# Kernel optimization log

Measured on AMD Instinct MI355X. Metric: run time of the kernel, lower is better.

## Reference

```python
import jax, jax.numpy as jnp
import numpy as np

N = 100000      # total nodes in batched graph
E = 3200000     # total edges (avg degree 32)
G = 128         # number of graphs in batch
F_IN = 512      # raw node feature dim
NC = 128        # num_classes = projected feature dim (GraphConv layer-0 input)
HID = 256       # hid_channels
OUT = 10        # out_channels
LYR = 3         # args.lyr
EPS = 1e-5      # BatchNorm1d eps


def setup_inputs() -> dict:
    key = jax.random.key(0)
    ks = jax.random.split(key, 20)
    h = jax.random.normal(ks[0], (N, F_IN), dtype=jnp.float32)
    src = jax.random.randint(ks[1], (E,), 0, N, dtype=jnp.int32)
    dst = jax.random.randint(ks[2], (E,), 0, N, dtype=jnp.int32)
    # contiguous sorted graph assignment: every graph non-empty
    graph_ids = (jnp.arange(N, dtype=jnp.int32) * G) // N
    w_init = jax.random.normal(ks[3], (NC, F_IN), dtype=jnp.float32) * 0.05
    inp = dict(h=h, src=src, dst=dst, graph_ids=graph_ids, w_init=w_init)
    dims = [NC, HID, HID]
    for i in range(LYR):
        inp[f"lw{i}"] = jax.random.normal(ks[4 + i], (dims[i], HID), dtype=jnp.float32) * 0.05
        inp[f"lb{i}"] = jnp.zeros((HID,), jnp.float32)
        inp[f"gamma{i}"] = jnp.ones((HID,), jnp.float32)
        inp[f"beta{i}"] = jnp.zeros((HID,), jnp.float32)
    inp["fc_w"] = jax.random.normal(ks[10], (HID, OUT), dtype=jnp.float32) * 0.05
    inp["fc_b"] = jnp.zeros((OUT,), jnp.float32)
    return inp


def _forward(h, src, dst, graph_ids, w_init, layers, fc_w, fc_b):
    # symmetric normalization (DGL GraphConv norm='both')
    ones_e = jnp.ones((E,), h.dtype)
    out_deg = jax.ops.segment_sum(ones_e, src, num_segments=N)
    in_deg = jax.ops.segment_sum(ones_e, dst, num_segments=N)
    norm_src = jnp.where(out_deg > 0, out_deg ** -0.5, 0.0)  # [N]
    norm_dst = jnp.where(in_deg > 0, in_deg ** -0.5, 0.0)    # [N]

    h = h @ w_init.T  # [N, NC]
    for (lw, lb, gamma, beta) in layers:
        # GraphConv: (D_out^-1/2) gather -> scatter-sum -> (D_in^-1/2), then linear
        m = (h * norm_src[:, None])[src]                       # [E, d]
        agg = jax.ops.segment_sum(m, dst, num_segments=N)       # [N, d]
        h = (agg * norm_dst[:, None]) @ lw + lb                 # [N, HID]
        # BatchNorm1d (training-mode batch stats, biased variance) + ReLU
        mu = jnp.mean(h, axis=0)
        var = jnp.mean((h - mu) ** 2, axis=0)
        h = jax.nn.relu((h - mu) * jax.lax.rsqrt(var + EPS) * gamma + beta)
    # dgl.max_nodes: per-graph max over nodes
    hg = jax.ops.segment_max(h, graph_ids, num_segments=G)      # [G, HID]
    return hg @ fc_w + fc_b                                     # [G, OUT]


def reference(h, src, dst, graph_ids, w_init,
              lw0, lb0, gamma0, beta0,
              lw1, lb1, gamma1, beta1,
              lw2, lb2, gamma2, beta2,
              fc_w, fc_b):
    layers = [(lw0, lb0, gamma0, beta0),
              (lw1, lb1, gamma1, beta1),
              (lw2, lb2, gamma2, beta2)]
    return _forward(h, src, dst, graph_ids, w_init, layers, fc_w, fc_b)
```

## Files before the change

kernel.cpp:

```cpp
#include <hip/hip_runtime.h>
#include <hip/hip_bf16.h>

#define N_NODES 100000
#define N_EDGES 3200000
#define N_GRAPHS 128
#define FIN 512
#define NCLS 128
#define HID 256
#define OUT_DIM 10
#define BN_EPS 1e-5f

#define NBUCK 391
#define EPB   ((N_EDGES + NBUCK - 1) / NBUCK)

typedef unsigned short ush;
typedef ush su16x8 __attribute__((ext_vector_type(8)));
typedef ush su16x4 __attribute__((ext_vector_type(4)));
typedef __bf16 bf16x8v __attribute__((ext_vector_type(8)));
typedef float f32x4v __attribute__((ext_vector_type(4)));

__device__ __forceinline__ float bf2f(ush u) {
    union { unsigned int i; float f; } v; v.i = ((unsigned int)u) << 16; return v.f;
}
__device__ __forceinline__ ush f2bf(float f) {
    union { float f; unsigned int i; } v; v.f = f;
    unsigned int r = v.i + 0x7FFFu + ((v.i >> 16) & 1u);
    return (ush)(r >> 16);
}

template <typename T>
__device__ __forceinline__ auto mfma_sel(T a, T b, f32x4v c, int)
    -> decltype(__builtin_amdgcn_mfma_f32_16x16x32_bf16(a, b, c, 0, 0, 0)) {
    return __builtin_amdgcn_mfma_f32_16x16x32_bf16(a, b, c, 0, 0, 0);
}
template <typename T>
__device__ __forceinline__ f32x4v mfma_sel(T a, T b, f32x4v c, long) {
    return __builtin_amdgcn_mfma_f32_16x16x32_bf16(
        __builtin_bit_cast(bf16x8v, a), __builtin_bit_cast(bf16x8v, b), c, 0, 0, 0);
}
__device__ __forceinline__ f32x4v MFMA_BF16(su16x8 a, su16x8 b, f32x4v c) {
    return mfma_sel(a, b, c, 0);
}

__global__ void odeg_kernel(const int* __restrict__ src, int* __restrict__ odeg8) {
    int e = blockIdx.x * 256 + threadIdx.x;
    int c = blockIdx.x & 7;
    if (e < N_EDGES) atomicAdd(&odeg8[(size_t)c * N_NODES + src[e]], 1);
}
__global__ void nsrc_kernel(const int* __restrict__ odeg8, float* __restrict__ nsrc) {
    int n = blockIdx.x * 256 + threadIdx.x;
    if (n < N_NODES) {
        int od = 0;
        #pragma unroll
        for (int c = 0; c < 8; c++) od += odeg8[(size_t)c * N_NODES + n];
        nsrc[n] = od > 0 ? rsqrtf((float)od) : 0.f;
    }
}

__global__ __launch_bounds__(256) void histA_kernel(const int* __restrict__ dst,
                                                    int* __restrict__ hist) {
    __shared__ int hc[NBUCK];
    int tid = threadIdx.x, blk = blockIdx.x;
    for (int i = tid; i < NBUCK; i += 256) hc[i] = 0;
    __syncthreads();
    int e0 = blk * EPB, e1 = e0 + EPB; if (e1 > N_EDGES) e1 = N_EDGES;
    for (int e = e0 + tid; e < e1; e += 256) atomicAdd(&hc[dst[e] >> 8], 1);
    __syncthreads();
    for (int i = tid; i < NBUCK; i += 256) hist[(size_t)blk * NBUCK + i] = hc[i];
}

__global__ __launch_bounds__(512) void bcnt_kernel(const int* __restrict__ hist,
                                                   int* __restrict__ bcnt) {
    __shared__ int ws[8];
    int b = blockIdx.x, tid = threadIdx.x;
    int lane = tid & 63, wid = tid >> 6;
    int v = (tid < NBUCK) ? hist[(size_t)tid * NBUCK + b] : 0;
    #pragma unroll
    for (int off = 32; off > 0; off >>= 1) v += __shfl_down(v, off, 64);
    if (lane == 0) ws[wid] = v;
    __syncthreads();
    if (tid == 0) {
        int s = 0;
        #pragma unroll
        for (int w = 0; w < 8; w++) s += ws[w];
        bcnt[b] = s;
    }
}

__global__ __launch_bounds__(512) void bscan_kernel(const int* __restrict__ bcnt,
                                                    int* __restrict__ bbase) {
    __shared__ int a[512];
    int tid = threadIdx.x;
    int v = (tid < NBUCK) ? bcnt[tid] : 0;
    a[tid] = v;
    __syncthreads();
    for (int s = 1; s < 512; s <<= 1) {
        int y = (tid >= s) ? a[tid - s] : 0;
        __syncthreads();
        a[tid] += y;
        __syncthreads();
    }
    if (tid < NBUCK) bbase[tid] = a[tid] - v;
    if (tid == 0) bbase[NBUCK] = N_EDGES;
}

__global__ __launch_bounds__(512) void boff_kernel(const int* __restrict__ hist,
                                                   const int* __restrict__ bbase,
                                                   int* __restrict__ off) {
    __shared__ int a[512];
    int b = blockIdx.x, tid = threadIdx.x;
    int v = (tid < NBUCK) ? hist[(size_t)tid * NBUCK + b] : 0;
    a[tid] = v;
    __syncthreads();
    for (int s = 1; s < 512; s <<= 1) {
        int y = (tid >= s) ? a[tid - s] : 0;
        __syncthreads();
        a[tid] += y;
        __syncthreads();
    }
    if (tid < NBUCK) off[(size_t)tid * NBUCK + b] = bbase[b] + a[tid] - v;
}

__global__ __launch_bounds__(256) void stage_kernel(const int* __restrict__ src,
                                                    const int* __restrict__ dst,
                                                    const int* __restrict__ off,
                                                    unsigned int* __restrict__ staged) {
    __shared__ int cur[NBUCK];
    int tid = threadIdx.x, blk = blockIdx.x;
    for (int i = tid; i < NBUCK; i += 256) cur[i] = off[(size_t)blk * NBUCK + i];
    __syncthreads();
    int e0 = blk * EPB, e1 = e0 + EPB; if (e1 > N_EDGES) e1 = N_EDGES;
    for (int e = e0 + tid; e < e1; e += 256) {
        int d = dst[e], s = src[e];
        int pos = atomicAdd(&cur[d >> 8], 1);
        staged[pos] = ((unsigned int)(d & 255) << 24) | (unsigned int)s;
    }
}

__global__ __launch_bounds__(256) void csr_kernel(const unsigned int* __restrict__ staged,
                                                  const int* __restrict__ bbase,
                                                  int* __restrict__ roff,
                                                  float* __restrict__ ndst,
                                                  int* __restrict__ csr) {
    __shared__ int cnt[256], pfx[256], cur[256];
    int b = blockIdx.x, tid = threadIdx.x;
    int beg = bbase[b], end = bbase[b + 1];
    int nodeBase = b * 256;
    int nNodes = N_NODES - nodeBase; if (nNodes > 256) nNodes = 256;
    cnt[tid] = 0;
    __syncthreads();
    for (int e = beg + tid; e < end; e += 256) atomicAdd(&cnt[staged[e] >> 24], 1);
    __syncthreads();
    int v = cnt[tid];
    pfx[tid] = v;
    __syncthreads();
    for (int s = 1; s < 256; s <<= 1) {
        int y = (tid >= s) ? pfx[tid - s] : 0;
        __syncthreads();
        pfx[tid] += y;
        __syncthreads();
    }
    int excl = pfx[tid] - v;
    pfx[tid] = excl;
    cur[tid] = 0;
    if (tid < nNodes) {
        int node = nodeBase + tid;
        roff[node] = beg + excl;
        ndst[node] = v > 0 ? rsqrtf((float)v) : 0.f;
    }
    if (b == NBUCK - 1 && tid == 0) roff[N_NODES] = N_EDGES;
    __syncthreads();
    for (int e = beg + tid; e < end; e += 256) {
        unsigned int w = staged[e];
        int dl = w >> 24;
        int pos = beg + pfx[dl] + atomicAdd(&cur[dl], 1);
        csr[pos] = (int)(w & 0xFFFFFFu);
    }
}

__global__ void cvt_w0_kernel(const float* __restrict__ w, ush* __restrict__ o) {
    int i = blockIdx.x * 256 + threadIdx.x;
    if (i < NCLS * FIN) o[i] = f2bf(w[i]);
}
__global__ void cvt_lwT_kernel(const float* __restrict__ lw, ush* __restrict__ o, int K) {
    int i = blockIdx.x * 256 + threadIdx.x;
    if (i < K * HID) {
        int n = i / K, k = i % K;
        o[i] = f2bf(lw[(size_t)k * HID + n]);
    }
}

template <bool A_F32, bool DO_STATS>
__global__ __launch_bounds__(256) void mfma_gemm(
    const void* __restrict__ Aptr, const ush* __restrict__ BT,
    ush* __restrict__ C, int M, int K, int NN,
    const float* __restrict__ rowscale, const float* __restrict__ bias,
    float* __restrict__ stats)
{
    __shared__ __align__(16) ush As[128][40];
    __shared__ __align__(16) ush Bs[128][40];
    const int bn0 = blockIdx.x * 128;
    const int bm0 = blockIdx.y * 128;
    const int tid = threadIdx.x;
    const int lane = tid & 63;
    const int wv = tid >> 6;
    const int wm = (wv >> 1) * 64;
    const int wn = (wv & 1) * 64;
    const int lm = lane & 15;
    const int lg = lane >> 4;

    f32x4v zero = {0.f, 0.f, 0.f, 0.f};
    f32x4v acc[4][4];
    #pragma unroll
    for (int mi = 0; mi < 4; mi++)
        #pragma unroll
        for (int ni = 0; ni < 4; ni++) acc[mi][ni] = zero;

    for (int k0 = 0; k0 < K; k0 += 32) {
        #pragma unroll
        for (int i = 0; i < 2; i++) {
            int seg = tid + i * 256;
            int n = seg >> 2, kp = seg & 3;
            su16x8 v = *(const su16x8*)&BT[(size_t)(bn0 + n) * K + k0 + kp * 8];
            *(su16x8*)&Bs[n][kp * 8] = v;
        }
        if constexpr (A_F32) {
            const float* Af = (const float*)Aptr;
            #pragma unroll
            for (int i = 0; i < 4; i++) {
                int seg = tid + i * 256;
                int m = seg >> 3, kp = seg & 7;
                int gm = bm0 + m; if (gm >= M) gm = M - 1;
                float4 v = *(const float4*)&Af[(size_t)gm * K + k0 + kp * 4];
                su16x4 o = { f2bf(v.x), f2bf(v.y), f2bf(v.z), f2bf(v.w) };
                *(su16x4*)&As[m][kp * 4] = o;
            }
        } else {
            const ush* Ab = (const ush*)Aptr;
            #pragma unroll
            for (int i = 0; i < 2; i++) {
                int seg = tid + i * 256;
                int m = seg >> 2, kp = seg & 3;
                int gm = bm0 + m; if (gm >= M) gm = M - 1;
                su16x8 v = *(const su16x8*)&Ab[(size_t)gm * K + k0 + kp * 8];
                *(su16x8*)&As[m][kp * 8] = v;
            }
        }
        __syncthreads();
        su16x8 af[4], bfr[4];
        #pragma unroll
        for (int i = 0; i < 4; i++)
            af[i] = *(const su16x8*)&As[wm + i * 16 + lm][lg * 8];
        #pragma unroll
        for (int i = 0; i < 4; i++)
            bfr[i] = *(const su16x8*)&Bs[wn + i * 16 + lm][lg * 8];
        #pragma unroll
        for (int mi = 0; mi < 4; mi++)
            #pragma unroll
            for (int ni = 0; ni < 4; ni++)
                acc[mi][ni] = MFMA_BF16(af[mi], bfr[ni], acc[mi][ni]);
        __syncthreads();
    }

    float s4[4] = {0.f, 0.f, 0.f, 0.f}, q4[4] = {0.f, 0.f, 0.f, 0.f};
    #pragma unroll
    for (int mi = 0; mi < 4; mi++) {
        #pragma unroll
        for (int j = 0; j < 4; j++) {
            int gm = bm0 + wm + mi * 16 + lg * 4 + j;
            bool valid = gm < M;
            float rs = (rowscale && valid) ? rowscale[gm] : 1.f;
            #pragma unroll
            for (int ni = 0; ni < 4; ni++) {
                int gn = bn0 + wn + ni * 16 + lm;
                float v = acc[mi][ni][j] * rs;
                if (bias) v += bias[gn];
                if (valid) {
                    C[(size_t)gm * NN + gn] = f2bf(v);
                    if constexpr (DO_STATS) { s4[ni] += v; q4[ni] += v * v; }
                }
            }
        }
    }
    if constexpr (DO_STATS) {
        #pragma unroll
        for (int ni = 0; ni < 4; ni++) {
            s4[ni] += __shfl_xor(s4[ni], 16); s4[ni] += __shfl_xor(s4[ni], 32);
            q4[ni] += __shfl_xor(q4[ni], 16); q4[ni] += __shfl_xor(q4[ni], 32);
        }
        if (lg == 0) {
            #pragma unroll
            for (int ni = 0; ni < 4; ni++) {
                int gn = bn0 + wn + ni * 16 + lm;
                atomicAdd(&stats[gn], s4[ni]);
                atomicAdd(&stats[HID + gn], q4[ni]);
            }
        }
    }
}

__global__ __launch_bounds__(256) void agg128(const ush* __restrict__ hs,
                                              const int* __restrict__ roff,
                                              const int* __restrict__ csr,
                                              ush* __restrict__ out)
{
    int node = (blockIdx.x * 256 + threadIdx.x) >> 6;
    int lane = threadIdx.x & 63;
    if (node >= N_NODES) return;
    int q = lane >> 4;
    int c0 = (lane & 15) * 8;
    int beg = roff[node], end = roff[node + 1];
    float accA[8] = {}, accB[8] = {};
    int e = beg + q;
    for (; e + 4 < end; e += 8) {
        int s0 = __builtin_nontemporal_load(&csr[e]);
        int s1 = __builtin_nontemporal_load(&csr[e + 4]);
        su16x8 v0 = *(const su16x8*)&hs[(size_t)s0 * 128 + c0];
        su16x8 v1 = *(const su16x8*)&hs[(size_t)s1 * 128 + c0];
        #pragma unroll
        for (int j = 0; j < 8; j++) { accA[j] += bf2f(v0[j]); accB[j] += bf2f(v1[j]); }
    }
    if (e < end) {
        int s0 = __builtin_nontemporal_load(&csr[e]);
        su16x8 v0 = *(const su16x8*)&hs[(size_t)s0 * 128 + c0];
        #pragma unroll
        for (int j = 0; j < 8; j++) accA[j] += bf2f(v0[j]);
    }
    #pragma unroll
    for (int j = 0; j < 8; j++) {
        accA[j] += accB[j];
        accA[j] += __shfl_xor(accA[j], 16);
        accA[j] += __shfl_xor(accA[j], 32);
    }
    if (lane < 16) {
        su16x8 o;
        #pragma unroll
        for (int j = 0; j < 8; j++) o[j] = f2bf(accA[j]);
        __builtin_nontemporal_store(o, (su16x8*)&out[(size_t)node * 128 + c0]);
    }
}

__global__ __launch_bounds__(256) void agg256(const ush* __restrict__ Q,
                                              const int* __restrict__ roff,
                                              const int* __restrict__ csr,
                                              ush* __restrict__ out)
{
    int node = (blockIdx.x * 256 + threadIdx.x) >> 6;
    int lane = threadIdx.x & 63;
    if (node >= N_NODES) return;
    int half = lane >> 5;
    int c0 = (lane & 31) * 8;
    int beg = roff[node], end = roff[node + 1];
    float accA[8] = {}, accB[8] = {};
    int e = beg + half;
    for (; e + 2 < end; e += 4) {
        int s0 = __builtin_nontemporal_load(&csr[e]);
        int s1 = __builtin_nontemporal_load(&csr[e + 2]);
        su16x8 v0 = *(const su16x8*)&Q[(size_t)s0 * 256 + c0];
        su16x8 v1 = *(const su16x8*)&Q[(size_t)s1 * 256 + c0];
        #pragma unroll
        for (int j = 0; j < 8; j++) { accA[j] += bf2f(v0[j]); accB[j] += bf2f(v1[j]); }
    }
    if (e < end) {
        int s0 = __builtin_nontemporal_load(&csr[e]);
        su16x8 v0 = *(const su16x8*)&Q[(size_t)s0 * 256 + c0];
        #pragma unroll
        for (int j = 0; j < 8; j++) accA[j] += bf2f(v0[j]);
    }
    #pragma unroll
    for (int j = 0; j < 8; j++) {
        accA[j] += accB[j];
        accA[j] += __shfl_xor(accA[j], 32);
    }
    if (lane < 32) {
        su16x8 o;
        #pragma unroll
        for (int j = 0; j < 8; j++) o[j] = f2bf(accA[j]);
        __builtin_nontemporal_store(o, (su16x8*)&out[(size_t)node * 256 + c0]);
    }
}

__global__ __launch_bounds__(256) void bnq_kernel(const ush* __restrict__ P,
                                                  const float* __restrict__ stats,
                                                  const float* __restrict__ gamma,
                                                  const float* __restrict__ beta,
                                                  const float* __restrict__ nsrc,
                                                  ush* __restrict__ Q)
{
    __shared__ float sa[HID], sb[HID];
    int tid = threadIdx.x;
    {
        const float inv_n = 1.f / (float)N_NODES;
        float mu = stats[tid] * inv_n;
        float var = fmaf(-mu, mu, stats[HID + tid] * inv_n);
        float a = gamma[tid] * rsqrtf(var + BN_EPS);
        sa[tid] = a;
        sb[tid] = fmaf(-mu, a, beta[tid]);
    }
    __syncthreads();
    const int total = N_NODES * 32;
    for (int idx = blockIdx.x * 256 + tid; idx < total; idx += gridDim.x * 256) {
        int r = idx >> 5, c0 = (idx & 31) * 8;
        su16x8 v = __builtin_nontemporal_load((const su16x8*)&P[(size_t)r * HID + c0]);
        float ns = nsrc[r];
        su16x8 o;
        #pragma unroll
        for (int j = 0; j < 8; j++) {
            float x = fmaxf(fmaf(bf2f(v[j]), sa[c0 + j], sb[c0 + j]), 0.f) * ns;
            o[j] = f2bf(x);
        }
        *(su16x8*)&Q[(size_t)r * HID + c0] = o;
    }
}

__global__ void gstart_kernel(const int* __restrict__ gids, int* __restrict__ gstart) {
    int n = blockIdx.x * 256 + threadIdx.x;
    if (n >= N_NODES) return;
    int g = gids[n];
    int gp = (n == 0) ? -1 : gids[n - 1];
    for (int gg = gp + 1; gg <= g; gg++) gstart[gg] = n;
    if (n == N_NODES - 1) {
        for (int gg = g + 1; gg <= N_GRAPHS; gg++) gstart[gg] = N_NODES;
    }
}

__global__ __launch_bounds__(256) void segmax_ab(const ush* __restrict__ pre,
                                                 const float* __restrict__ stats,
                                                 const float* __restrict__ gamma,
                                                 const float* __restrict__ beta,
                                                 const int* __restrict__ gstart,
                                                 float* __restrict__ hg) {
    int c = threadIdx.x;
    const float inv_n = 1.f / (float)N_NODES;
    float mu = stats[c] * inv_n;
    float var = fmaf(-mu, mu, stats[HID + c] * inv_n);
    float a = gamma[c] * rsqrtf(var + BN_EPS);
    float b = fmaf(-mu, a, beta[c]);
    int g = blockIdx.x;
    int chunk = blockIdx.y;
    int beg = gstart[g], end = gstart[g + 1];
    int len = end - beg;
    int per = (len + 7) >> 3;
    int s = beg + chunk * per;
    int e = s + per; if (e > end) e = end;
    float m0 = 0.f, m1 = 0.f;
    int n = s;
    for (; n + 1 < e; n += 2) {
        m0 = fmaxf(m0, fmaf(bf2f(pre[(size_t)n * HID + c]), a, b));
        m1 = fmaxf(m1, fmaf(bf2f(pre[(size_t)(n + 1) * HID + c]), a, b));
    }
    if (n < e) m0 = fmaxf(m0, fmaf(bf2f(pre[(size_t)n * HID + c]), a, b));
    float m = fmaxf(fmaxf(m0, m1), 0.f);
    atomicMax((int*)&hg[g * HID + c], __float_as_int(m));
}

__global__ void fc_kernel(const float* __restrict__ hg, const float* __restrict__ w,
                          const float* __restrict__ b, float* __restrict__ out) {
    int idx = blockIdx.x * 256 + threadIdx.x;
    if (idx >= N_GRAPHS * OUT_DIM) return;
    int g = idx / OUT_DIM, j = idx % OUT_DIM;
    float s = b[j];
    for (int c = 0; c < HID; c++) s += hg[g * HID + c] * w[c * OUT_DIM + j];
    out[idx] = s;
}

extern "C" void kernel_launch(void* const* d_in, const int* in_sizes, int n_in,
                              void* d_out, int out_size, void* d_ws, size_t ws_size,
                              hipStream_t stream) {
    const float* h      = (const float*)d_in[0];
    const int*   src    = (const int*)d_in[1];
    const int*   dst    = (const int*)d_in[2];
    const int*   gids   = (const int*)d_in[3];
    const float* w_init = (const float*)d_in[4];
    const float* lw[3]    = { (const float*)d_in[5],  (const float*)d_in[9],  (const float*)d_in[13] };
    const float* lb[3]    = { (const float*)d_in[6],  (const float*)d_in[10], (const float*)d_in[14] };
    const float* gamma[3] = { (const float*)d_in[7],  (const float*)d_in[11], (const float*)d_in[15] };
    const float* beta[3]  = { (const float*)d_in[8],  (const float*)d_in[12], (const float*)d_in[16] };
    const float* fc_w = (const float*)d_in[17];
    const float* fc_b = (const float*)d_in[18];
    float* out = (float*)d_out;

    char* ws = (char*)d_ws;
    size_t off_b = 0;
    auto alloc = [&](size_t bytes) { size_t o = off_b; off_b += (bytes + 255) & ~(size_t)255; return o; };
    size_t o_h0s   = alloc((size_t)N_NODES * NCLS * 2);
    size_t o_aggb  = alloc((size_t)N_NODES * HID * 2);
    size_t o_P     = alloc((size_t)N_NODES * HID * 2);
    size_t o_Q     = alloc((size_t)N_NODES * HID * 2);
    size_t o_wB0   = alloc((size_t)NCLS * FIN * 2);
    size_t o_lwT0  = alloc((size_t)HID * NCLS * 2);
    size_t o_lwT1  = alloc((size_t)HID * HID * 2);
    size_t o_lwT2  = alloc((size_t)HID * HID * 2);
    size_t o_nsrc  = alloc((size_t)N_NODES * 4);
    size_t o_ndst  = alloc((size_t)N_NODES * 4);
    size_t o_odeg8 = alloc((size_t)8 * N_NODES * 4);
    size_t o_roff  = alloc((size_t)(N_NODES + 1) * 4);
    size_t o_csr   = alloc((size_t)N_EDGES * 4);
    size_t o_stg   = alloc((size_t)N_EDGES * 4);
    size_t o_hist  = alloc((size_t)NBUCK * NBUCK * 4);
    size_t o_off   = alloc((size_t)NBUCK * NBUCK * 4);
    size_t o_bcnt  = alloc((size_t)(NBUCK + 1) * 4);
    size_t o_bbase = alloc((size_t)(NBUCK + 1) * 4);
    size_t o_stats = alloc((size_t)3 * 2 * HID * 4);
    size_t o_gst   = alloc((size_t)(N_GRAPHS + 1) * 4);
    size_t o_hg    = alloc((size_t)N_GRAPHS * HID * 4);
    if (off_b > ws_size) return;

    ush*   h0s  = (ush*)(ws + o_h0s);
    ush*   aggb = (ush*)(ws + o_aggb);
    ush*   P    = (ush*)(ws + o_P);
    ush*   Q    = (ush*)(ws + o_Q);
    ush*   wB0  = (ush*)(ws + o_wB0);
    ush*   lwT[3] = { (ush*)(ws + o_lwT0), (ush*)(ws + o_lwT1), (ush*)(ws + o_lwT2) };
    float* nsrc = (float*)(ws + o_nsrc);
    float* ndst = (float*)(ws + o_ndst);
    int*   odeg8= (int*)(ws + o_odeg8);
    int*   roff = (int*)(ws + o_roff);
    int*   csr  = (int*)(ws + o_csr);
    unsigned int* stg = (unsigned int*)(ws + o_stg);
    int*   hist = (int*)(ws + o_hist);
    int*   boff = (int*)(ws + o_off);
    int*   bcnt = (int*)(ws + o_bcnt);
    int*   bbase= (int*)(ws + o_bbase);
    float* stats= (float*)(ws + o_stats);
    int*   gst  = (int*)(ws + o_gst);
    float* hg   = (float*)(ws + o_hg);

    const int eb = (N_EDGES + 255) / 256;
    const int nb = (N_NODES + 255) / 256;

    hipMemsetAsync(odeg8, 0, (size_t)8 * N_NODES * 4, stream);
    hipMemsetAsync(stats, 0, 3 * 2 * HID * 4, stream);
    hipMemsetAsync(hg, 0, (size_t)N_GRAPHS * HID * 4, stream);

    odeg_kernel<<<eb, 256, 0, stream>>>(src, odeg8);
    nsrc_kernel<<<nb, 256, 0, stream>>>(odeg8, nsrc);

    histA_kernel<<<NBUCK, 256, 0, stream>>>(dst, hist);
    bcnt_kernel<<<NBUCK, 512, 0, stream>>>(hist, bcnt);
    bscan_kernel<<<1, 512, 0, stream>>>(bcnt, bbase);
    boff_kernel<<<NBUCK, 512, 0, stream>>>(hist, bbase, boff);
    stage_kernel<<<NBUCK, 256, 0, stream>>>(src, dst, boff, stg);
    csr_kernel<<<NBUCK, 256, 0, stream>>>(stg, bbase, roff, ndst, csr);

    gstart_kernel<<<nb, 256, 0, stream>>>(gids, gst);

    cvt_w0_kernel<<<(NCLS * FIN + 255) / 256, 256, 0, stream>>>(w_init, wB0);
    cvt_lwT_kernel<<<(NCLS * HID + 255) / 256, 256, 0, stream>>>(lw[0], lwT[0], NCLS);
    cvt_lwT_kernel<<<(HID * HID + 255) / 256, 256, 0, stream>>>(lw[1], lwT[1], HID);
    cvt_lwT_kernel<<<(HID * HID + 255) / 256, 256, 0, stream>>>(lw[2], lwT[2], HID);

    const int mblocks = (N_NODES + 127) / 128;
    const int aggblocks = (N_NODES * 64 + 255) / 256;

    {
        dim3 grid(NCLS / 128, mblocks);
        mfma_gemm<true, false><<<grid, 256, 0, stream>>>(h, wB0, h0s, N_NODES, FIN, NCLS,
                                                         nsrc, nullptr, nullptr);
    }

    agg128<<<aggblocks, 256, 0, stream>>>(h0s, roff, csr, aggb);
    {
        dim3 grid(HID / 128, mblocks);
        mfma_gemm<false, true><<<grid, 256, 0, stream>>>(aggb, lwT[0], P, N_NODES, NCLS, HID,
                                                         ndst, lb[0], stats);
    }

    for (int l = 1; l < 3; l++) {
        bnq_kernel<<<1024, 256, 0, stream>>>(P, stats + (l - 1) * 2 * HID,
                                             gamma[l - 1], beta[l - 1], nsrc, Q);
        agg256<<<aggblocks, 256, 0, stream>>>(Q, roff, csr, aggb);
        dim3 grid(HID / 128, mblocks);
        mfma_gemm<false, true><<<grid, 256, 0, stream>>>(aggb, lwT[l], P, N_NODES, HID, HID,
                                                         ndst, lb[l], stats + l * 2 * HID);
    }

    {
        dim3 grid(N_GRAPHS, 8);
        segmax_ab<<<grid, 256, 0, stream>>>(P, stats + 2 * 2 * HID, gamma[2], beta[2], gst, hg);
    }
    fc_kernel<<<(N_GRAPHS * OUT_DIM + 255) / 256, 256, 0, stream>>>(hg, fc_w, fc_b, out);
}
```

Measured before the change: 1.174 ms.

## Fuse edge degree/histogram passes, merge weight casts, restructure aggregation edge split

Merges the out-degree atomic pass and the destination-bucket histogram into one edge kernel so src and dst are read in a single launch. The four weight conversion kernels become one launch. The aggregation kernels now give each lane group a contiguous chunk of the neighbour list, with 4 independent accumulators and 4 gathers in flight, replacing strided 2-way unrolling and dropping nontemporal hints on csr. The fused edge kernel uses only 391 blocks for the global atomics, so it may lose parallelism compared with the former per-256-edge grid.

```diff
diff --git a/kernel.cpp b/kernel.cpp
--- a/kernel.cpp
+++ b/kernel.cpp
@@ -42,11 +42,24 @@
     return mfma_sel(a, b, c, 0);
 }
 
-__global__ void odeg_kernel(const int* __restrict__ src, int* __restrict__ odeg8) {
-    int e = blockIdx.x * 256 + threadIdx.x;
-    int c = blockIdx.x & 7;
-    if (e < N_EDGES) atomicAdd(&odeg8[(size_t)c * N_NODES + src[e]], 1);
-}
+__global__ __launch_bounds__(256) void edge_pass1(const int* __restrict__ src,
+                                                  const int* __restrict__ dst,
+                                                  int* __restrict__ odeg8,
+                                                  int* __restrict__ hist) {
+    __shared__ int hc[NBUCK];
+    int tid = threadIdx.x, blk = blockIdx.x;
+    for (int i = tid; i < NBUCK; i += 256) hc[i] = 0;
+    __syncthreads();
+    int e0 = blk * EPB, e1 = e0 + EPB; if (e1 > N_EDGES) e1 = N_EDGES;
+    int c = blk & 7;
+    for (int e = e0 + tid; e < e1; e += 256) {
+        atomicAdd(&odeg8[(size_t)c * N_NODES + src[e]], 1);
+        atomicAdd(&hc[dst[e] >> 8], 1);
+    }
+    __syncthreads();
+    for (int i = tid; i < NBUCK; i += 256) hist[(size_t)blk * NBUCK + i] = hc[i];
+}
+
 __global__ void nsrc_kernel(const int* __restrict__ odeg8, float* __restrict__ nsrc) {
     int n = blockIdx.x * 256 + threadIdx.x;
     if (n < N_NODES) {
@@ -55,18 +68,6 @@
         for (int c = 0; c < 8; c++) od += odeg8[(size_t)c * N_NODES + n];
         nsrc[n] = od > 0 ? rsqrtf((float)od) : 0.f;
     }
-}
-
-__global__ __launch_bounds__(256) void histA_kernel(const int* __restrict__ dst,
-                                                    int* __restrict__ hist) {
-    __shared__ int hc[NBUCK];
-    int tid = threadIdx.x, blk = blockIdx.x;
-    for (int i = tid; i < NBUCK; i += 256) hc[i] = 0;
-    __syncthreads();
-    int e0 = blk * EPB, e1 = e0 + EPB; if (e1 > N_EDGES) e1 = N_EDGES;
-    for (int e = e0 + tid; e < e1; e += 256) atomicAdd(&hc[dst[e] >> 8], 1);
-    __syncthreads();
-    for (int i = tid; i < NBUCK; i += 256) hist[(size_t)blk * NBUCK + i] = hc[i];
 }
 
 __global__ __launch_bounds__(512) void bcnt_kernel(const int* __restrict__ hist,
@@ -178,17 +179,20 @@
     }
 }
 
-__global__ void cvt_w0_kernel(const float* __restrict__ w, ush* __restrict__ o) {
+__global__ void cvt_weights(const float* __restrict__ w0, const float* __restrict__ l0,
+                            const float* __restrict__ l1, const float* __restrict__ l2,
+                            ush* __restrict__ wB0, ush* __restrict__ t0,
+                            ush* __restrict__ t1, ush* __restrict__ t2) {
     int i = blockIdx.x * 256 + threadIdx.x;
-    if (i < NCLS * FIN) o[i] = f2bf(w[i]);
-}
-__global__ void cvt_lwT_kernel(const float* __restrict__ lw, ush* __restrict__ o, int K) {
-    int i = blockIdx.x * 256 + threadIdx.x;
-    if (i < K * HID) {
-        int n = i / K, k = i % K;
-        o[i] = f2bf(lw[(size_t)k * HID + n]);
-    }
-}
+    if (i < NCLS * FIN) { wB0[i] = f2bf(w0[i]); return; }
+    i -= NCLS * FIN;
+    if (i < HID * NCLS) { int n = i >> 7, k = i & 127; t0[i] = f2bf(l0[k * HID + n]); return; }
+    i -= HID * NCLS;
+    if (i < HID * HID) { int n = i >> 8, k = i & 255; t1[i] = f2bf(l1[k * HID + n]); return; }
+    i -= HID * HID;
+    if (i < HID * HID) { int n = i >> 8, k = i & 255; t2[i] = f2bf(l2[k * HID + n]); }
+}
+#define CVT_TOTAL (NCLS * FIN + HID * NCLS + HID * HID + HID * HID)
 
 template <bool A_F32, bool DO_STATS>
 __global__ __launch_bounds__(256) void mfma_gemm(
@@ -310,32 +314,39 @@
     int q = lane >> 4;
     int c0 = (lane & 15) * 8;
     int beg = roff[node], end = roff[node + 1];
-    float accA[8] = {}, accB[8] = {};
-    int e = beg + q;
-    for (; e + 4 < end; e += 8) {
-        int s0 = __builtin_nontemporal_load(&csr[e]);
-        int s1 = __builtin_nontemporal_load(&csr[e + 4]);
-        su16x8 v0 = *(const su16x8*)&hs[(size_t)s0 * 128 + c0];
-        su16x8 v1 = *(const su16x8*)&hs[(size_t)s1 * 128 + c0];
-        #pragma unroll
-        for (int j = 0; j < 8; j++) { accA[j] += bf2f(v0[j]); accB[j] += bf2f(v1[j]); }
-    }
-    if (e < end) {
-        int s0 = __builtin_nontemporal_load(&csr[e]);
-        su16x8 v0 = *(const su16x8*)&hs[(size_t)s0 * 128 + c0];
-        #pragma unroll
-        for (int j = 0; j < 8; j++) accA[j] += bf2f(v0[j]);
+    int len = end - beg;
+    int s = beg + ((len * q) >> 2);
+    int t = beg + ((len * (q + 1)) >> 2);
+    float a0[8] = {}, a1[8] = {}, a2[8] = {}, a3[8] = {};
+    int e = s;
+    for (; e + 3 < t; e += 4) {
+        int i0 = csr[e], i1 = csr[e + 1], i2 = csr[e + 2], i3 = csr[e + 3];
+        su16x8 v0 = *(const su16x8*)&hs[(size_t)i0 * 128 + c0];
+        su16x8 v1 = *(const su16x8*)&hs[(size_t)i1 * 128 + c0];
+        su16x8 v2 = *(const su16x8*)&hs[(size_t)i2 * 128 + c0];
+        su16x8 v3 = *(const su16x8*)&hs[(size_t)i3 * 128 + c0];
+        #pragma unroll
+        for (int j = 0; j < 8; j++) {
+            a0[j] += bf2f(v0[j]); a1[j] += bf2f(v1[j]);
+            a2[j] += bf2f(v2[j]); a3[j] += bf2f(v3[j]);
+        }
+    }
+    for (; e < t; e++) {
+        int i0 = csr[e];
+        su16x8 v0 = *(const su16x8*)&hs[(size_t)i0 * 128 + c0];
+        #pragma unroll
+        for (int j = 0; j < 8; j++) a0[j] += bf2f(v0[j]);
     }
     #pragma unroll
     for (int j = 0; j < 8; j++) {
-        accA[j] += accB[j];
-        accA[j] += __shfl_xor(accA[j], 16);
-        accA[j] += __shfl_xor(accA[j], 32);
+        a0[j] += a1[j] + a2[j] + a3[j];
+        a0[j] += __shfl_xor(a0[j], 16);
+        a0[j] += __shfl_xor(a0[j], 32);
     }
     if (lane < 16) {
         su16x8 o;
         #pragma unroll
-        for (int j = 0; j < 8; j++) o[j] = f2bf(accA[j]);
+        for (int j = 0; j < 8; j++) o[j] = f2bf(a0[j]);
         __builtin_nontemporal_store(o, (su16x8*)&out[(size_t)node * 128 + c0]);
     }
 }
@@ -351,31 +362,38 @@
     int half = lane >> 5;
     int c0 = (lane & 31) * 8;
     int beg = roff[node], end = roff[node + 1];
-    float accA[8] = {}, accB[8] = {};
-    int e = beg + half;
-    for (; e + 2 < end; e += 4) {
-        int s0 = __builtin_nontemporal_load(&csr[e]);
-        int s1 = __builtin_nontemporal_load(&csr[e + 2]);
-        su16x8 v0 = *(const su16x8*)&Q[(size_t)s0 * 256 + c0];
-        su16x8 v1 = *(const su16x8*)&Q[(size_t)s1 * 256 + c0];
-        #pragma unroll
-        for (int j = 0; j < 8; j++) { accA[j] += bf2f(v0[j]); accB[j] += bf2f(v1[j]); }
-    }
-    if (e < end) {
-        int s0 = __builtin_nontemporal_load(&csr[e]);
-        su16x8 v0 = *(const su16x8*)&Q[(size_t)s0 * 256 + c0];
-        #pragma unroll
-        for (int j = 0; j < 8; j++) accA[j] += bf2f(v0[j]);
+    int len = end - beg;
+    int s = beg + ((len * half) >> 1);
+    int t = beg + ((len * (half + 1)) >> 1);
+    float a0[8] = {}, a1[8] = {}, a2[8] = {}, a3[8] = {};
+    int e = s;
+    for (; e + 3 < t; e += 4) {
+        int i0 = csr[e], i1 = csr[e + 1], i2 = csr[e + 2], i3 = csr[e + 3];
+        su16x8 v0 = *(const su16x8*)&Q[(size_t)i0 * 256 + c0];
+        su16x8 v1 = *(const su16x8*)&Q[(size_t)i1 * 256 + c0];
+        su16x8 v2 = *(const su16x8*)&Q[(size_t)i2 * 256 + c0];
+        su16x8 v3 = *(const su16x8*)&Q[(size_t)i3 * 256 + c0];
+        #pragma unroll
+        for (int j = 0; j < 8; j++) {
+            a0[j] += bf2f(v0[j]); a1[j] += bf2f(v1[j]);
+            a2[j] += bf2f(v2[j]); a3[j] += bf2f(v3[j]);
+        }
+    }
+    for (; e < t; e++) {
+        int i0 = csr[e];
+        su16x8 v0 = *(const su16x8*)&Q[(size_t)i0 * 256 + c0];
+        #pragma unroll
+        for (int j = 0; j < 8; j++) a0[j] += bf2f(v0[j]);
     }
     #pragma unroll
     for (int j = 0; j < 8; j++) {
-        accA[j] += accB[j];
-        accA[j] += __shfl_xor(accA[j], 32);
+        a0[j] += a1[j] + a2[j] + a3[j];
+        a0[j] += __shfl_xor(a0[j], 32);
     }
     if (lane < 32) {
         su16x8 o;
         #pragma unroll
-        for (int j = 0; j < 8; j++) o[j] = f2bf(accA[j]);
+        for (int j = 0; j < 8; j++) o[j] = f2bf(a0[j]);
         __builtin_nontemporal_store(o, (su16x8*)&out[(size_t)node * 256 + c0]);
     }
 }
@@ -526,17 +544,15 @@
     int*   gst  = (int*)(ws + o_gst);
     float* hg   = (float*)(ws + o_hg);
 
-    const int eb = (N_EDGES + 255) / 256;
     const int nb = (N_NODES + 255) / 256;
 
     hipMemsetAsync(odeg8, 0, (size_t)8 * N_NODES * 4, stream);
     hipMemsetAsync(stats, 0, 3 * 2 * HID * 4, stream);
     hipMemsetAsync(hg, 0, (size_t)N_GRAPHS * HID * 4, stream);
 
-    odeg_kernel<<<eb, 256, 0, stream>>>(src, odeg8);
+    edge_pass1<<<NBUCK, 256, 0, stream>>>(src, dst, odeg8, hist);
     nsrc_kernel<<<nb, 256, 0, stream>>>(odeg8, nsrc);
 
-    histA_kernel<<<NBUCK, 256, 0, stream>>>(dst, hist);
     bcnt_kernel<<<NBUCK, 512, 0, stream>>>(hist, bcnt);
     bscan_kernel<<<1, 512, 0, stream>>>(bcnt, bbase);
     boff_kernel<<<NBUCK, 512, 0, stream>>>(hist, bbase, boff);
@@ -545,10 +561,8 @@
 
     gstart_kernel<<<nb, 256, 0, stream>>>(gids, gst);
 
-    cvt_w0_kernel<<<(NCLS * FIN + 255) / 256, 256, 0, stream>>>(w_init, wB0);
-    cvt_lwT_kernel<<<(NCLS * HID + 255) / 256, 256, 0, stream>>>(lw[0], lwT[0], NCLS);
-    cvt_lwT_kernel<<<(HID * HID + 255) / 256, 256, 0, stream>>>(lw[1], lwT[1], HID);
-    cvt_lwT_kernel<<<(HID * HID + 255) / 256, 256, 0, stream>>>(lw[2], lwT[2], HID);
+    cvt_weights<<<(CVT_TOTAL + 255) / 256, 256, 0, stream>>>(w_init, lw[0], lw[1], lw[2],
+                                                             wB0, lwT[0], lwT[1], lwT[2]);
 
     const int mblocks = (N_NODES + 127) / 128;
     const int aggblocks = (N_NODES * 64 + 255) / 256;
```

New measurement: 1.124 ms. 4.3% less time.
